# Performance work log

Measured on AMD Instinct MI355X. Metric: run time of the kernel, lower is better.

## Reference

```python
import jax, jax.numpy as jnp
import numpy as np

NUM_EMBEDDINGS = 1024
EMBEDDING_DIM = 256
COMMITMENT_COST = 0.25


def setup_inputs() -> dict:
    key = jax.random.key(0)
    k1, k2 = jax.random.split(key)
    x = jax.random.normal(k1, (32, 256, 32, 32), dtype=jnp.float32)
    # torch init: uniform(-1/K, 1/K)
    lim = 1.0 / NUM_EMBEDDINGS
    codebook = jax.random.uniform(k2, (NUM_EMBEDDINGS, EMBEDDING_DIM), dtype=jnp.float32,
                                  minval=-lim, maxval=lim)
    return {"x": x, "codebook": codebook}


def reference(x, codebook):
    B, C, H, W = x.shape
    K = codebook.shape[0]
    inputs = jnp.transpose(x, (0, 2, 3, 1))          # [B,H,W,C]
    flat = inputs.reshape(-1, C)                     # [N,C]
    N = flat.shape[0]

    # squared euclidean distance via matmul expansion
    distances = (jnp.sum(flat * flat, axis=1, keepdims=True)
                 + jnp.sum(codebook * codebook, axis=1)
                 - 2.0 * flat @ codebook.T)          # [N,K]
    idx = jnp.argmin(distances, axis=1)              # [N]

    # gather lookup (same math as one-hot @ codebook)
    quantized = codebook[idx].reshape(inputs.shape)  # [B,H,W,C]

    sg = jax.lax.stop_gradient
    e_latent_loss = jnp.mean((sg(quantized) - inputs) ** 2)
    q_latent_loss = jnp.mean((quantized - sg(inputs)) ** 2)
    loss = q_latent_loss + COMMITMENT_COST * e_latent_loss

    quantized_st = inputs + sg(quantized - inputs)   # straight-through

    # avg one-hot probs via bincount-style scatter-add
    counts = jnp.zeros((K,), dtype=jnp.float32).at[idx].add(1.0)
    avg_probs = counts / N
    perplexity = jnp.exp(-jnp.sum(avg_probs * jnp.log(avg_probs + 1e-10)))

    q_out = jnp.transpose(quantized_st, (0, 3, 1, 2))  # back to NCHW
    return loss, q_out, perplexity, idx.reshape(B, H, W)
```

## Files before the change

### kernel.cpp

```cpp
#include <hip/hip_runtime.h>
#include <math.h>

#define K_    1024
#define N_    32768
#define NELEM 8388608

#define Q_OFF    1
#define PERP_OFF 8388609
#define IDX_OFF  8388610

#define XLO_F_OFF 4

typedef unsigned long long ull;
typedef _Float16 h8  __attribute__((ext_vector_type(8)));
typedef float    f4v __attribute__((ext_vector_type(4)));

#define WS_COUNTS  0
#define WS_SUMSQ   4096
#define WS_RISKCNT 4104
#define WS_DONE    4108
#define WS_EN2     4160
#define WS_XN2     8256
#define WS_IDX     139328
#define WS_RLIST   270400
#define WS_RKEY    401472
#define WS_EHI     663616
#define WS_XHI     1187904

#define RISKY_Q 207u

__device__ __forceinline__ unsigned u32min(unsigned a, unsigned b) { return a < b ? a : b; }
__device__ __forceinline__ unsigned u32max(unsigned a, unsigned b) { return a > b ? a : b; }

__device__ __forceinline__ void vmem_drain() {
    asm volatile("s_waitcnt vmcnt(0)" ::: "memory");
}

__global__ __launch_bounds__(256) void k_pre(const float* __restrict__ x,
                                             const float* __restrict__ cb,
                                             ushort* __restrict__ xfh,
                                             ushort* __restrict__ xfl,
                                             float* __restrict__ xn2,
                                             ushort* __restrict__ efh,
                                             float* __restrict__ en2,
                                             ull* __restrict__ rkey,
                                             unsigned* __restrict__ counts,
                                             unsigned* __restrict__ rcnt,
                                             unsigned* __restrict__ done,
                                             double* __restrict__ sumsq) {
    __shared__ float T[256 * 68];
    __shared__ double red[256];
    const int t = threadIdx.x, bid = blockIdx.x;

    if (bid < 512) {
        const int b = bid >> 4, hw0 = (bid & 15) << 6;
        const float* xb = x + b * 262144 + hw0;
#pragma unroll
        for (int i = 0; i < 16; ++i) {
            const int jv = i * 256 + t, c = jv >> 4, p4 = (jv & 15) << 2;
            const int sw = ((c >> 3) & 3) << 3;
            *(float4*)(&T[c * 68 + (p4 ^ sw)]) = *(const float4*)(xb + c * 1024 + p4);
        }
        __syncthreads();
        const int mi = t >> 6, lane = t & 63;
        const int quad = (t >> 4) & 3, l15 = t & 15;
        const int pxs = (mi * 16 + l15) ^ (quad << 3);
        double sn = 0.0;
        const size_t obase = (size_t)bid * 16384 + lane * 8;
#pragma unroll
        for (int dc = 0; dc < 8; ++dc) {
            union { _Float16 h[8]; int4 v; } ph, pl;
#pragma unroll
            for (int j = 0; j < 8; ++j) {
                const float v = T[(dc * 32 + quad * 8 + j) * 68 + pxs];
                sn += (double)v * v;
                const _Float16 hi = (_Float16)v;
                ph.h[j] = hi;
                pl.h[j] = (_Float16)((v - (float)hi) * 2048.0f);
            }
            *(int4*)(xfh + obase + (dc * 4 + mi) * 512) = ph.v;
            *(int4*)(xfl + obase + (dc * 4 + mi) * 512) = pl.v;
        }
        red[t] = sn;
        __syncthreads();
        if (t < 64) {
            const int base = (t >> 4) * 64 + (t & 15);
            xn2[bid * 64 + t] = (float)(red[base] + red[base + 16] +
                                        red[base + 32] + red[base + 48]);
        }
    } else if (bid < 528) {
        const int n = (bid - 512) * 64 + (t >> 2);
        const int seg = t & 3;
        const float* src = cb + (size_t)n * 256 + seg * 64;
        const int kt = n >> 8, wch = (n >> 6) & 3, ci = (n >> 4) & 3, l15 = n & 15;
        double s = 0.0;
#pragma unroll
        for (int g = 0; g < 8; ++g) {
            const float4 a = *(const float4*)(src + g * 8);
            const float4 b = *(const float4*)(src + g * 8 + 4);
            s += (double)a.x * a.x + (double)a.y * a.y + (double)a.z * a.z + (double)a.w * a.w;
            s += (double)b.x * b.x + (double)b.y * b.y + (double)b.z * b.z + (double)b.w * b.w;
            const float v[8] = {a.x, a.y, a.z, a.w, b.x, b.y, b.z, b.w};
            union { _Float16 h[8]; int4 q; } ph;
#pragma unroll
            for (int j = 0; j < 8; ++j)
                ph.h[j] = (_Float16)(v[j] * 1024.0f);
            const int dc = seg * 2 + (g >> 2);
            const int quad = g & 3;
            const size_t addr = ((size_t)(((kt * 4 + wch) * 8 + dc) * 4 + ci) * 64 +
                                 (quad * 16 + l15)) * 8;
            *(int4*)(efh + addr) = ph.q;
        }
        red[t] = s;
        __syncthreads();
        if (t < 64) {
            const int r2 = (bid - 512) * 64 + t;
            en2[r2] = (float)(red[t * 4] + red[t * 4 + 1] + red[t * 4 + 2] + red[t * 4 + 3]);
        }
    } else {
        const int ib = bid - 528;
        const int i0 = ib * 512 + t * 2;
        rkey[i0] = ~0ull; rkey[i0 + 1] = ~0ull;
        if (ib == 0) {
            ((uint4*)counts)[t] = make_uint4(0u, 0u, 0u, 0u);
            if (t == 0) { *rcnt = 0u; *done = 0u; *sumsq = 0.0; }
        }
    }
}

__global__ __launch_bounds__(256, 2) void k_sweep(const ushort* __restrict__ xfh,
                                                  const ushort* __restrict__ xfl,
                                                  const ushort* __restrict__ efh,
                                                  const float* __restrict__ en2,
                                                  int* __restrict__ idxv,
                                                  int* __restrict__ rlist,
                                                  unsigned* __restrict__ rcnt) {
    __shared__ __align__(16) ushort Bsh[16384];
    __shared__ __align__(16) ushort Bsl[16384];
    __shared__ __align__(16) float  enS[1024];
    __shared__ unsigned Mg[4][64][2];

    const int t = threadIdx.x, bid = blockIdx.x;
    const int p0 = bid << 6;
    const int w = t >> 6, lane = t & 63;
    const int quad = lane >> 4, l15 = lane & 15;

    {
        const size_t base = (size_t)bid * 16384;
#pragma unroll
        for (int i = 0; i < 8; ++i) {
            const int off = (i * 256 + t) * 8;
            *(int4*)(&Bsh[off]) = *(const int4*)(xfh + base + off);
            *(int4*)(&Bsl[off]) = *(const int4*)(xfl + base + off);
        }
#pragma unroll
        for (int i = 0; i < 4; ++i)
            enS[i * 256 + t] = en2[i * 256 + t] * 1024.0f;
    }
    __syncthreads();

    unsigned K1[4], K2[4];
#pragma unroll
    for (int ni = 0; ni < 4; ++ni) { K1[ni] = 0xFFFFFFFFu; K2[ni] = 0xFFFFFFFFu; }

    for (int kt = 0; kt < 4; ++kt) {
        const f4v z = {0.f, 0.f, 0.f, 0.f};
        f4v acc1[4][4], acc2[4][4];
#pragma unroll
        for (int mi = 0; mi < 4; ++mi)
#pragma unroll
            for (int ni = 0; ni < 4; ++ni) { acc1[mi][ni] = z; acc2[mi][ni] = z; }

#pragma unroll 2
        for (int dc = 0; dc < 8; ++dc) {
            h8 ah[4], bh[4], bl[4];
            const size_t abase = ((size_t)((kt * 4 + w) * 8 + dc) * 4) * 512 + lane * 8;
#pragma unroll
            for (int mi = 0; mi < 4; ++mi)
                ah[mi] = *(const h8*)(efh + abase + mi * 512);
            const int bbase = dc * 2048 + lane * 8;
#pragma unroll
            for (int ni = 0; ni < 4; ++ni) {
                bh[ni] = *(const h8*)(&Bsh[bbase + ni * 512]);
                bl[ni] = *(const h8*)(&Bsl[bbase + ni * 512]);
            }
#pragma unroll
            for (int mi = 0; mi < 4; ++mi)
#pragma unroll
                for (int ni = 0; ni < 4; ++ni) {
                    acc1[mi][ni] = __builtin_amdgcn_mfma_f32_16x16x32_f16(
                        ah[mi], bh[ni], acc1[mi][ni], 0, 0, 0);
                    acc2[mi][ni] = __builtin_amdgcn_mfma_f32_16x16x32_f16(
                        ah[mi], bl[ni], acc2[mi][ni], 0, 0, 0);
                }
        }
#pragma unroll
        for (int mi = 0; mi < 4; ++mi) {
            const int cbase = kt * 256 + w * 64 + mi * 16 + quad * 4;
            const f4v en4 = *(const f4v*)(&enS[cbase]);
#pragma unroll
            for (int ni = 0; ni < 4; ++ni) {
#pragma unroll
                for (int r = 0; r < 4; ++r) {
                    const float cmb = acc1[mi][ni][r] + acc2[mi][ni][r] * (1.0f / 2048.0f);
                    const float dist = fmaf(-2.0f, cmb, en4[r]);
                    float qf = fmaf(dist, 1024.0f, 131072.0f);
                    qf = fminf(fmaxf(qf, 0.0f), 524287.0f);
                    const unsigned key = ((unsigned)(int)qf << 10) | (unsigned)(cbase + r);
                    const unsigned o1 = K1[ni];
                    K1[ni] = u32min(o1, key);
                    K2[ni] = u32min(K2[ni], u32max(o1, key));
                }
            }
        }
    }
#pragma unroll
    for (int m = 16; m <= 32; m <<= 1) {
#pragma unroll
        for (int ni = 0; ni < 4; ++ni) {
            const unsigned a1 = (unsigned)__shfl_xor((int)K1[ni], m, 64);
            const unsigned a2 = (unsigned)__shfl_xor((int)K2[ni], m, 64);
            const unsigned n1 = u32min(K1[ni], a1);
            const unsigned n2 = u32min(u32max(K1[ni], a1), u32min(K2[ni], a2));
            K1[ni] = n1; K2[ni] = n2;
        }
    }
    if (quad == 0) {
#pragma unroll
        for (int ni = 0; ni < 4; ++ni) {
            Mg[w][ni * 16 + l15][0] = K1[ni];
            Mg[w][ni * 16 + l15][1] = K2[ni];
        }
    }
    __syncthreads();
    if (t < 64) {
        unsigned b1 = Mg[0][t][0], b2 = Mg[0][t][1];
#pragma unroll
        for (int ww = 1; ww < 4; ++ww) {
            const unsigned a1 = Mg[ww][t][0], a2 = Mg[ww][t][1];
            const unsigned n1 = u32min(b1, a1);
            b2 = u32min(u32max(b1, a1), u32min(b2, a2));
            b1 = n1;
        }
        const int P = p0 + t;
        idxv[P] = (int)(b1 & 1023u);
        const bool risky = ((b2 >> 10) - (b1 >> 10)) <= RISKY_Q;
        const ull mask = __ballot(risky);
        const int pre = __popcll(mask & ((1ull << t) - 1ull));
        unsigned base = 0;
        if (t == 0) base = atomicAdd(rcnt, (unsigned)__popcll(mask));
        base = (unsigned)__shfl((int)base, 0, 64);
        if (risky) rlist[base + pre] = P;
    }
}

__global__ __launch_bounds__(256) void k_rescan(const float* __restrict__ x,
                                                const float* __restrict__ cb,
                                                const float* __restrict__ en2,
                                                const float* __restrict__ xn2,
                                                const int* __restrict__ rlist,
                                                const unsigned* __restrict__ rcnt,
                                                ull* __restrict__ rkey) {
    __shared__ float xs[64 * 68];
    __shared__ float es[64 * 132];
    __shared__ int plist[64];
    const int t = threadIdx.x;
    const unsigned cnt = *rcnt;
    const int nunits = (int)(((cnt + 63) >> 6) << 3);
    const int ti = t >> 4, tj = t & 15;

    for (int u = blockIdx.x; u < nunits; u += gridDim.x) {
        const int tile = u >> 3, kt = u & 7;
        __syncthreads();
        if (t < 64) {
            const int li = tile * 64 + t;
            plist[t] = rlist[li < (int)cnt ? li : 0];
        }
        __syncthreads();

        float xnr[4]; int pid[4];
#pragma unroll
        for (int r = 0; r < 4; ++r) {
            pid[r] = plist[ti * 4 + r];
            xnr[r] = xn2[pid[r]];
        }
        float acc[4][8];
#pragma unroll
        for (int r = 0; r < 4; ++r)
#pragma unroll
            for (int j = 0; j < 8; ++j) acc[r][j] = 0.f;
        float best_s[4]; int best_k[4];
#pragma unroll
        for (int r = 0; r < 4; ++r) { best_s[r] = INFINITY; best_k[r] = 0; }

        for (int dc = 0; dc < 4; ++dc) {
            __syncthreads();
            {
                const int p = t & 63, coff = t >> 6;
                const int P = plist[p];
                const float* xp = x + ((P >> 10) * 262144 + (P & 1023));
#pragma unroll
                for (int cc = 0; cc < 16; ++cc) {
                    const int cl = coff * 16 + cc;
                    xs[cl * 68 + p] = xp[(dc * 64 + cl) * 1024];
                }
            }
#pragma unroll
            for (int i = 0; i < 8; ++i) {
                const int jv = i * 256 + t, k = jv >> 4, d4 = (jv & 15) << 2;
                const float4 v = *(const float4*)(cb + (size_t)(kt * 128 + k) * 256 + dc * 64 + d4);
                es[(d4 + 0) * 132 + k] = v.x; es[(d4 + 1) * 132 + k] = v.y;
                es[(d4 + 2) * 132 + k] = v.z; es[(d4 + 3) * 132 + k] = v.w;
            }
            __syncthreads();
#pragma unroll 4
            for (int d = 0; d < 64; ++d) {
                const float4 xv = *(const float4*)(&xs[d * 68 + ti * 4]);
                const float4 e0 = *(const float4*)(&es[d * 132 + tj * 8]);
                const float4 e1 = *(const float4*)(&es[d * 132 + tj * 8 + 4]);
                const float xr[4] = {xv.x, xv.y, xv.z, xv.w};
                const float ej[8] = {e0.x, e0.y, e0.z, e0.w, e1.x, e1.y, e1.z, e1.w};
#pragma unroll
                for (int r = 0; r < 4; ++r)
#pragma unroll
                    for (int j = 0; j < 8; ++j)
                        acc[r][j] = fmaf(xr[r], ej[j], acc[r][j]);
            }
        }
#pragma unroll
        for (int j = 0; j < 8; ++j) {
            const int k = kt * 128 + tj * 8 + j;
            const float en = en2[k];
#pragma unroll
            for (int r = 0; r < 4; ++r) {
                const float s1 = xnr[r] + en;
                const float dist = fmaf(-2.f, acc[r][j], s1);
                if (dist < best_s[r] || (dist == best_s[r] && k < best_k[r])) {
                    best_s[r] = dist; best_k[r] = k;
                }
            }
        }
#pragma unroll
        for (int r = 0; r < 4; ++r) {
            float s = best_s[r]; int k = best_k[r];
            for (int m = 1; m < 16; m <<= 1) {
                const float s2 = __shfl_xor(s, m, 64);
                const int k2 = __shfl_xor(k, m, 64);
                if (s2 < s || (s2 == s && k2 < k)) { s = s2; k = k2; }
            }
            if (tj == 0 && (tile * 64 + ti * 4 + r) < (int)cnt) {
                const ull key = ((ull)__float_as_uint(s) << 32) | (unsigned)k;
                atomicMin(&rkey[pid[r]], key);
            }
        }
    }
}

__global__ __launch_bounds__(256) void k_gather(const float* __restrict__ x,
                                                const float* __restrict__ cb,
                                                const int* __restrict__ idxv,
                                                const ull* __restrict__ rkey,
                                                float* __restrict__ out,
                                                double* __restrict__ psum,
                                                unsigned* __restrict__ counts,
                                                unsigned* __restrict__ done) {
    __shared__ __align__(16) float cs[32 * 260];
    __shared__ int   kidx[32];
    __shared__ float wpart[4];
    __shared__ int   lastf;
    __shared__ double part[256];
    __shared__ double part2[256];

    const int t = threadIdx.x, bid = blockIdx.x;
    const int n0 = bid * 32;
    if (t < 32) {
        const int n = n0 + t;
        const ull rk = rkey[n];
        const int kk = (rk != ~0ull) ? (int)(unsigned)(rk & 0xffffffffu) : idxv[n];
        kidx[t] = kk;
        atomicAdd(&counts[kk], 1u);
        out[IDX_OFF + n] = (float)kk;
    }
    if (t == 0) lastf = 0;
    __syncthreads();
#pragma unroll
    for (int i = 0; i < 8; ++i) {
        int jv = (i << 8) + t;
        int p = jv >> 6, c4 = (jv & 63) << 2;
        const float4 v = *(const float4*)(cb + (size_t)kidx[p] * 256 + c4);
        *(float4*)(&cs[p * 260 + c4]) = v;
    }
    __syncthreads();

    const int b = bid >> 5, h = bid & 31;
    const float* xb = x + b * 262144 + h * 32;
    float* qb = out + Q_OFF + b * 262144 + h * 32;

    float local = 0.f;
#pragma unroll
    for (int i = 0; i < 8; ++i) {
        int j = (i << 8) + t;
        int c = j >> 3, w4 = (j & 7) << 2;
        const float q0 = cs[(w4 + 0) * 260 + c];
        const float q1 = cs[(w4 + 1) * 260 + c];
        const float q2 = cs[(w4 + 2) * 260 + c];
        const float q3 = cs[(w4 + 3) * 260 + c];
        const float4 xv = *(const float4*)(xb + c * 1024 + w4);
        const float d0 = q0 - xv.x, d1 = q1 - xv.y;
        const float d2 = q2 - xv.z, d3 = q3 - xv.w;
        local += d0 * d0 + d1 * d1 + d2 * d2 + d3 * d3;
        qb[c * 1024 + w4 + 0] = q0;
        qb[c * 1024 + w4 + 1] = q1;
        qb[c * 1024 + w4 + 2] = q2;
        qb[c * 1024 + w4 + 3] = q3;
    }
    for (int m = 32; m > 0; m >>= 1) local += __shfl_down(local, m, 64);
    if ((t & 63) == 0) wpart[t >> 6] = local;
    __syncthreads();
    if (t == 0) {
        const double bs = (double)wpart[0] + (double)wpart[1] +
                          (double)wpart[2] + (double)wpart[3];
        atomicExch((ull*)&psum[bid], (ull)__double_as_longlong(bs));
        vmem_drain();
        if (atomicAdd(done, 1u) == 1023u) lastf = 1;
    }
    __syncthreads();
    if (lastf) {
        double s = 0.0, ss = 0.0;
        for (int k = t; k < K_; k += 256) {
            const unsigned c = atomicAdd(&counts[k], 0u);
            const double p = (double)c / (double)N_;
            s += p * log(p + 1e-10);
        }
#pragma unroll
        for (int i = 0; i < 4; ++i) {
            const ull pv = atomicAdd((ull*)&psum[i * 256 + t], 0ull);
            ss += __longlong_as_double((long long)pv);
        }
        part[t] = s; part2[t] = ss;
        __syncthreads();
        for (int off = 128; off > 0; off >>= 1) {
            if (t < off) { part[t] += part[t + off]; part2[t] += part2[t + off]; }
            __syncthreads();
        }
        if (t == 0) {
            out[PERP_OFF] = (float)exp(-part[0]);
            out[0] = (float)(part2[0] * 1.25 / (double)NELEM);
        }
    }
}

extern "C" void kernel_launch(void* const* d_in, const int* in_sizes, int n_in,
                              void* d_out, int out_size, void* d_ws, size_t ws_size,
                              hipStream_t stream) {
    const float* x  = (const float*)d_in[0];
    const float* cb = (const float*)d_in[1];
    float* out = (float*)d_out;
    char*  ws  = (char*)d_ws;

    unsigned* counts = (unsigned*)(ws + WS_COUNTS);
    double*   sumsq  = (double*)(ws + WS_SUMSQ);
    unsigned* rcnt   = (unsigned*)(ws + WS_RISKCNT);
    unsigned* done   = (unsigned*)(ws + WS_DONE);
    float*    en2    = (float*)(ws + WS_EN2);
    float*    xn2    = (float*)(ws + WS_XN2);
    int*      idxv   = (int*)(ws + WS_IDX);
    int*      rlist  = (int*)(ws + WS_RLIST);
    ull*      rkey   = (ull*)(ws + WS_RKEY);
    ushort*   efh    = (ushort*)(ws + WS_EHI);
    ushort*   xfh    = (ushort*)(ws + WS_XHI);
    ushort*   xfl    = (ushort*)(out + XLO_F_OFF);
    double*   psum   = (double*)(ws + WS_RLIST);

    k_pre<<<592, 256, 0, stream>>>(x, cb, xfh, xfl, xn2, efh, en2,
                                   rkey, counts, rcnt, done, sumsq);
    k_sweep<<<512, 256, 0, stream>>>(xfh, xfl, efh, en2, idxv, rlist, rcnt);
    k_rescan<<<512, 256, 0, stream>>>(x, cb, en2, xn2, rlist, rcnt, rkey);
    k_gather<<<1024, 256, 0, stream>>>(x, cb, idxv, rkey, out, psum, counts, done);
}
```

Before: 205.7 us.

## Stage risky pixels' fp32 rows in sweep scratch for coalesced rescan loads

At the end of k_sweep, each block reloads the full fp32 channel vectors of its risky pixels from NCHW x. It writes them as contiguous 256-float rows into the now-dead fp16 hi/lo scratch buffers. k_rescan then reads these rows with float4 loads instead of doing strided 1024-element gathers per channel. The codebook transpose tile stride is also changed from 132 to 133 to reduce LDS bank conflicts. This adds strided reads inside sweep and reuses the xfh/xfl buffers, which must no longer be needed after sweep.

```diff
diff --git a/kernel.cpp b/kernel.cpp
--- a/kernel.cpp
+++ b/kernel.cpp
@@ -26,6 +26,8 @@
 #define WS_RKEY    401472
 #define WS_EHI     663616
 #define WS_XHI     1187904
+
+#define ES_LD 133
 
 #define RISKY_Q 207u
 
@@ -128,8 +130,9 @@
     }
 }
 
-__global__ __launch_bounds__(256, 2) void k_sweep(const ushort* __restrict__ xfh,
-                                                  const ushort* __restrict__ xfl,
+__global__ __launch_bounds__(256, 2) void k_sweep(const float* __restrict__ x,
+                                                  ushort* __restrict__ xfh,
+                                                  ushort* __restrict__ xfl,
                                                   const ushort* __restrict__ efh,
                                                   const float* __restrict__ en2,
                                                   int* __restrict__ idxv,
@@ -139,6 +142,8 @@
     __shared__ __align__(16) ushort Bsl[16384];
     __shared__ __align__(16) float  enS[1024];
     __shared__ unsigned Mg[4][64][2];
+    __shared__ int rpixS[64];
+    __shared__ int rnS;
 
     const int t = threadIdx.x, bid = blockIdx.x;
     const int p0 = bid << 6;
@@ -248,13 +253,34 @@
         const ull mask = __ballot(risky);
         const int pre = __popcll(mask & ((1ull << t) - 1ull));
         unsigned base = 0;
-        if (t == 0) base = atomicAdd(rcnt, (unsigned)__popcll(mask));
+        if (t == 0) { base = atomicAdd(rcnt, (unsigned)__popcll(mask)); rnS = (int)__popcll(mask); }
         base = (unsigned)__shfl((int)base, 0, 64);
-        if (risky) rlist[base + pre] = P;
+        if (risky) { rlist[base + pre] = P; rpixS[pre] = t; }
+    }
+    __syncthreads();
+    {
+        const int rn = rnS;
+        float* xth = (float*)(xfh + (size_t)bid * 16384);
+        float* xtl = (float*)(xfl + (size_t)bid * 16384);
+        for (int i = w; i < rn; i += 4) {
+            const int lp = rpixS[i];
+            const int P = p0 + lp;
+            const float* xp = x + (size_t)(P >> 10) * 262144 + (P & 1023);
+            const int c0 = lane * 4;
+            float4 vv;
+            vv.x = xp[(size_t)(c0 + 0) * 1024];
+            vv.y = xp[(size_t)(c0 + 1) * 1024];
+            vv.z = xp[(size_t)(c0 + 2) * 1024];
+            vv.w = xp[(size_t)(c0 + 3) * 1024];
+            float* dst = (c0 < 128) ? (xth + lp * 128 + c0)
+                                    : (xtl + lp * 128 + (c0 - 128));
+            *(float4*)dst = vv;
+        }
     }
 }
 
-__global__ __launch_bounds__(256) void k_rescan(const float* __restrict__ x,
+__global__ __launch_bounds__(256) void k_rescan(const float* __restrict__ xth,
+                                                const float* __restrict__ xtl,
                                                 const float* __restrict__ cb,
                                                 const float* __restrict__ en2,
                                                 const float* __restrict__ xn2,
@@ -262,7 +288,7 @@
                                                 const unsigned* __restrict__ rcnt,
                                                 ull* __restrict__ rkey) {
     __shared__ float xs[64 * 68];
-    __shared__ float es[64 * 132];
+    __shared__ float es[64 * ES_LD];
     __shared__ int plist[64];
     const int t = threadIdx.x;
     const unsigned cnt = *rcnt;
@@ -298,26 +324,33 @@
             {
                 const int p = t & 63, coff = t >> 6;
                 const int P = plist[p];
-                const float* xp = x + ((P >> 10) * 262144 + (P & 1023));
-#pragma unroll
-                for (int cc = 0; cc < 16; ++cc) {
-                    const int cl = coff * 16 + cc;
-                    xs[cl * 68 + p] = xp[(dc * 64 + cl) * 1024];
+                const size_t rbase = (size_t)(P >> 6) * 8192 + (size_t)(P & 63) * 128;
+                const int c0 = dc * 64 + coff * 16;
+                const float* src = (c0 < 128) ? (xth + rbase + c0)
+                                              : (xtl + rbase + (c0 - 128));
+#pragma unroll
+                for (int q = 0; q < 4; ++q) {
+                    const float4 v = *(const float4*)(src + q * 4);
+                    const int cl = coff * 16 + q * 4;
+                    xs[(cl + 0) * 68 + p] = v.x;
+                    xs[(cl + 1) * 68 + p] = v.y;
+                    xs[(cl + 2) * 68 + p] = v.z;
+                    xs[(cl + 3) * 68 + p] = v.w;
                 }
             }
 #pragma unroll
             for (int i = 0; i < 8; ++i) {
                 const int jv = i * 256 + t, k = jv >> 4, d4 = (jv & 15) << 2;
                 const float4 v = *(const float4*)(cb + (size_t)(kt * 128 + k) * 256 + dc * 64 + d4);
-                es[(d4 + 0) * 132 + k] = v.x; es[(d4 + 1) * 132 + k] = v.y;
-                es[(d4 + 2) * 132 + k] = v.z; es[(d4 + 3) * 132 + k] = v.w;
+                es[(d4 + 0) * ES_LD + k] = v.x; es[(d4 + 1) * ES_LD + k] = v.y;
+                es[(d4 + 2) * ES_LD + k] = v.z; es[(d4 + 3) * ES_LD + k] = v.w;
             }
             __syncthreads();
 #pragma unroll 4
             for (int d = 0; d < 64; ++d) {
                 const float4 xv = *(const float4*)(&xs[d * 68 + ti * 4]);
-                const float4 e0 = *(const float4*)(&es[d * 132 + tj * 8]);
-                const float4 e1 = *(const float4*)(&es[d * 132 + tj * 8 + 4]);
+                const float4 e0 = *(const float4*)(&es[d * ES_LD + tj * 8]);
+                const float4 e1 = *(const float4*)(&es[d * ES_LD + tj * 8 + 4]);
                 const float xr[4] = {xv.x, xv.y, xv.z, xv.w};
                 const float ej[8] = {e0.x, e0.y, e0.z, e0.w, e1.x, e1.y, e1.z, e1.w};
 #pragma unroll
@@ -474,7 +507,8 @@
 
     k_pre<<<592, 256, 0, stream>>>(x, cb, xfh, xfl, xn2, efh, en2,
                                    rkey, counts, rcnt, done, sumsq);
-    k_sweep<<<512, 256, 0, stream>>>(xfh, xfl, efh, en2, idxv, rlist, rcnt);
-    k_rescan<<<512, 256, 0, stream>>>(x, cb, en2, xn2, rlist, rcnt, rkey);
+    k_sweep<<<512, 256, 0, stream>>>(x, xfh, xfl, efh, en2, idxv, rlist, rcnt);
+    k_rescan<<<512, 256, 0, stream>>>((const float*)xfh, (const float*)xfl,
+                                      cb, en2, xn2, rlist, rcnt, rkey);
     k_gather<<<1024, 256, 0, stream>>>(x, cb, idxv, rkey, out, psum, counts, done);
 }
```

Result: faster. 192.8 us (-6.3%).
